# Kernel tuning notes

Measured on AMD Instinct MI355X. Metric: run time of the kernel, lower is better.

The kernel has to match this reference:

```python
import jax, jax.numpy as jnp
import numpy as np

# Config constants (match init_kwargs)
D_MODEL = 1024
N_EXPERTS = 8
EXPERT_SCALE = 2          # experts per base group -> n_base_groups = 4
N_FEAT = 16
BANK_DIM = 32
RAW_FEAT = N_FEAT * BANK_DIM   # 512
PROJ_DIM = 256
R_HIDDEN = 256
E_HIDDEN = 256
TOP_K = 2
TEMP = 1.0
LN_EPS = 1e-5


def _layernorm(x, g, b):
    mu = jnp.mean(x, axis=-1, keepdims=True)
    var = jnp.mean((x - mu) ** 2, axis=-1, keepdims=True)
    return (x - mu) * jax.lax.rsqrt(var + LN_EPS) * g + b


def _softmax_top_k(logits, k):
    # keep top-k logits, mask rest to -inf, softmax
    topv = jax.lax.top_k(logits, k)[0]
    thresh = topv[..., -1:]
    masked = jnp.where(logits >= thresh, logits, -jnp.inf)
    return jax.nn.softmax(masked, axis=-1)


def setup_inputs() -> dict:
    key = jax.random.key(0)
    ks = jax.random.split(key, 24)
    B, S = 4, 2048
    s = 0.02
    inp = {
        "hidden": jax.random.normal(ks[0], (B, S, D_MODEL), jnp.float32),
        "feat": jax.random.normal(ks[1], (B, S, N_FEAT), jnp.float32),
        "feat_bank": jax.random.normal(ks[2], (B, S, N_FEAT, BANK_DIM), jnp.float32),
        "item_seq_len": jax.random.randint(ks[3], (B,), 1, S + 1, jnp.int64),
        # pre-LN
        "ln_g": jnp.ones((D_MODEL,), jnp.float32),
        "ln_b": jnp.zeros((D_MODEL,), jnp.float32),
        # router feature projector (2 layers: Linear -> GELU -> Linear)
        "fp_w1": jax.random.normal(ks[4], (RAW_FEAT, PROJ_DIM), jnp.float32) * s,
        "fp_b1": jnp.zeros((PROJ_DIM,), jnp.float32),
        "fp_w2": jax.random.normal(ks[5], (PROJ_DIM, PROJ_DIM), jnp.float32) * s,
        "fp_b2": jnp.zeros((PROJ_DIM,), jnp.float32),
        # learned router MLP: d_in = d_model + proj_dim
        "r_w1": jax.random.normal(ks[6], (D_MODEL + PROJ_DIM, R_HIDDEN), jnp.float32) * s,
        "r_b1": jnp.zeros((R_HIDDEN,), jnp.float32),
        "r_w2": jax.random.normal(ks[7], (R_HIDDEN, N_EXPERTS), jnp.float32) * s,
        "r_b2": jnp.zeros((N_EXPERTS,), jnp.float32),
        # rule router (linear on raw stage features)
        "rr_w": jax.random.normal(ks[8], (N_FEAT, N_EXPERTS), jnp.float32) * s,
        "rr_b": jnp.zeros((N_EXPERTS,), jnp.float32),
        # per-expert FFN
        "e_w1": jax.random.normal(ks[9], (N_EXPERTS, D_MODEL, E_HIDDEN), jnp.float32) * s,
        "e_b1": jnp.zeros((N_EXPERTS, E_HIDDEN), jnp.float32),
        "e_w2": jax.random.normal(ks[10], (N_EXPERTS, E_HIDDEN, D_MODEL), jnp.float32) * s,
        "e_b2": jnp.zeros((N_EXPERTS, D_MODEL), jnp.float32),
        "alpha": jnp.ones((), jnp.float32),
    }
    return inp


def reference(hidden, feat, feat_bank, item_seq_len, ln_g, ln_b,
              fp_w1, fp_b1, fp_w2, fp_b2,
              r_w1, r_b1, r_w2, r_b2,
              rr_w, rr_b,
              e_w1, e_b1, e_w2, e_b2, alpha):
    B, S, D = hidden.shape
    h_norm = _layernorm(hidden, ln_g, ln_b)  # [B,S,D]

    # router feature path: flatten bank, 2-layer GELU projector
    bank_flat = feat_bank.reshape(B, S, RAW_FEAT)
    proj = jnp.dot(jax.nn.gelu(jnp.dot(bank_flat, fp_w1) + fp_b1), fp_w2) + fp_b2  # [B,S,P]

    # token-mode router input: concat hidden + projected features
    router_input = jnp.concatenate([h_norm, proj], axis=-1)
    rule_logits = jnp.dot(feat, rr_w) + rr_b  # rule router on raw stage features

    raw_logits = jnp.dot(jax.nn.gelu(jnp.dot(router_input, r_w1) + r_b1), r_w2) + r_b2
    scaled_logits = raw_logits / max(TEMP, 1e-6)
    gate_weights = _softmax_top_k(scaled_logits, TOP_K)           # [B,S,E]
    rule_target_logits = rule_logits / max(TEMP, 1e-6)

    # expert group: per-expert 2-layer GELU FFN on h_norm
    h1 = jax.nn.gelu(jnp.einsum('bsd,edh->bseh', h_norm, e_w1) + e_b1)
    expert_out = jnp.einsum('bseh,ehd->bsed', h1, e_w2) + e_b2    # [B,S,E,D]

    stage_out = jnp.einsum('bse,bsed->bsd', gate_weights, expert_out)
    next_hidden = hidden + alpha * stage_out

    # _aggregate_group_weights: expert_group_idx = arange(E)//EXPERT_SCALE is
    # contiguous, so gather+sum per group == reshape+sum over the scale axis
    n_groups = N_EXPERTS // EXPERT_SCALE
    group_weights = gate_weights.reshape(B, S, n_groups, EXPERT_SCALE).sum(-1)

    return (next_hidden, stage_out, gate_weights, scaled_logits, group_weights, rule_target_logits)
```

## Files before the change

kernel.cpp:

```cpp
#include <hip/hip_runtime.h>
#include <stdint.h>


typedef unsigned short u16;
using bf16x8 = __attribute__((ext_vector_type(8))) short;
using f32x4  = __attribute__((ext_vector_type(4))) float;

#define WS_HHI 0u
#define WS_HLO 16777216u
#define WS_PB2 33554432u
#define WS_W1T 67108864u
#define WS_IDX 71303168u
#define IX_SELE   0u
#define IX_SELG   65536u
#define IX_ROW    131072u
#define IX_TOKR   196608u
#define IX_GROW   262144u
#define IX_CNT    327680u
#define IX_CBASE  335872u
#define IX_TILEE  344064u
#define IX_TILES  344704u
#define IX_TILEC  345344u
#define IX_META   345984u
#define IX_TILEE2 346112u
#define IX_TILES2 347264u
#define IX_TILEC2 348416u

__device__ __forceinline__ float gelu_tanh(float x) {
  float x3 = x * x * x;
  float t = tanhf(0.7978845608028654f * (x + 0.044715f * x3));
  return 0.5f * x * (1.0f + t);
}
__device__ __forceinline__ u16 f2bf(float f) {
  uint32_t u = __float_as_uint(f);
  u = u + 0x7fffu + ((u >> 16) & 1u);
  return (u16)(u >> 16);
}
__device__ __forceinline__ float b2f(u16 h) {
  return __uint_as_float(((uint32_t)h) << 16);
}
__device__ __forceinline__ void gll16(const void* g, void* l) {
  __builtin_amdgcn_global_load_lds(
      (const __attribute__((address_space(1))) void*)g,
      (__attribute__((address_space(3))) void*)l, 16, 0, 0);
}

__global__ __launch_bounds__(256) void split_bank_kernel(const float* __restrict__ x,
    u16* __restrict__ hi, u16* __restrict__ lo) {
  int i4 = blockIdx.x * 256 + threadIdx.x;
  float4 v = ((const float4*)x)[i4];
  ushort4 h, l;
  h.x = f2bf(v.x); l.x = f2bf(v.x - b2f(h.x));
  h.y = f2bf(v.y); l.y = f2bf(v.y - b2f(h.y));
  h.z = f2bf(v.z); l.z = f2bf(v.z - b2f(h.z));
  h.w = f2bf(v.w); l.w = f2bf(v.w - b2f(h.w));
  ((ushort4*)hi)[i4] = h;
  ((ushort4*)lo)[i4] = l;
}

__global__ __launch_bounds__(256) void tsplit_kernel(const float* __restrict__ in,
    int inR, int inC, u16* __restrict__ outHi, u16* __restrict__ outLo,
    int outLD, int outColOff) {
  __shared__ u16 hs[64][65];
  __shared__ u16 ls[64][65];
  int tid = threadIdx.x;
  int c0 = blockIdx.x * 64, r0 = blockIdx.y * 64;
  const float* inp = in + (size_t)blockIdx.z * inR * inC;
  int rl = tid >> 6, cl = tid & 63;
#pragma unroll
  for (int p = 0; p < 16; p++) {
    int r = rl + p * 4;
    float v = inp[(size_t)(r0 + r) * inC + c0 + cl];
    u16 h = f2bf(v);
    hs[r][cl] = h;
    ls[r][cl] = f2bf(v - b2f(h));
  }
  __syncthreads();
  size_t obase = (size_t)(blockIdx.z * inC + c0) * outLD + outColOff + r0;
#pragma unroll
  for (int p = 0; p < 16; p++) {
    int c = rl + p * 4;
    outHi[obase + (size_t)c * outLD + cl] = hs[cl][c];
    if (outLo) outLo[obase + (size_t)c * outLD + cl] = ls[cl][c];
  }
}

__global__ __launch_bounds__(256) void wprime_kernel(const float* __restrict__ fp_w2,
    const float* __restrict__ r_w1, const float* __restrict__ fp_b2,
    const float* __restrict__ r_b1, float* __restrict__ wp, float* __restrict__ bp) {
  __shared__ float row[256];
  int i = blockIdx.x, n = threadIdx.x;
  if (i < 256) {
    row[n] = fp_w2[i * 256 + n];
    __syncthreads();
    float acc = 0.0f;
    for (int j = 0; j < 256; j++) acc += row[j] * r_w1[(size_t)(1024 + j) * 256 + n];
    wp[i * 256 + n] = acc;
  } else {
    row[n] = fp_b2[n];
    __syncthreads();
    float acc = r_b1[n];
    for (int j = 0; j < 256; j++) acc += row[j] * r_w1[(size_t)(1024 + j) * 256 + n];
    bp[n] = acc;
  }
}

__global__ __launch_bounds__(256) void ln_kernel(const float* __restrict__ hidden,
    const float* __restrict__ ln_g, const float* __restrict__ ln_b,
    const float* __restrict__ feat, const float* __restrict__ rr_w,
    const float* __restrict__ rr_b,
    u16* __restrict__ h_hi, u16* __restrict__ h_lo, float* __restrict__ rule) {
  int t = blockIdx.x;
  int tid = threadIdx.x;
  float4 v = ((const float4*)(hidden + (size_t)t * 1024))[tid];
  float s = v.x + v.y + v.z + v.w;
#pragma unroll
  for (int o = 32; o > 0; o >>= 1) s += __shfl_down(s, o);
  __shared__ float red[4];
  __shared__ float stats[2];
  int wid = tid >> 6, lane = tid & 63;
  if (lane == 0) red[wid] = s;
  __syncthreads();
  if (tid == 0) stats[0] = (red[0] + red[1] + red[2] + red[3]) * (1.0f / 1024.0f);
  __syncthreads();
  float mu = stats[0];
  float dx = v.x - mu, dy = v.y - mu, dz = v.z - mu, dw = v.w - mu;
  float q = dx * dx + dy * dy + dz * dz + dw * dw;
#pragma unroll
  for (int o = 32; o > 0; o >>= 1) q += __shfl_down(q, o);
  if (lane == 0) red[wid] = q;
  __syncthreads();
  if (tid == 0) {
    float var = (red[0] + red[1] + red[2] + red[3]) * (1.0f / 1024.0f) + 1e-5f;
    float r = rsqrtf(var);
    r = r * (1.5f - 0.5f * var * r * r);
    stats[1] = r;
  }
  __syncthreads();
  float r = stats[1];
  float4 g = ((const float4*)ln_g)[tid];
  float4 b = ((const float4*)ln_b)[tid];
  float4 o;
  o.x = dx * r * g.x + b.x;
  o.y = dy * r * g.y + b.y;
  o.z = dz * r * g.z + b.z;
  o.w = dw * r * g.w + b.w;
  ushort4 hv, lv;
  hv.x = f2bf(o.x); lv.x = f2bf(o.x - b2f(hv.x));
  hv.y = f2bf(o.y); lv.y = f2bf(o.y - b2f(hv.y));
  hv.z = f2bf(o.z); lv.z = f2bf(o.z - b2f(hv.z));
  hv.w = f2bf(o.w); lv.w = f2bf(o.w - b2f(hv.w));
  ((ushort4*)(h_hi + (size_t)t * 1024))[tid] = hv;
  ((ushort4*)(h_lo + (size_t)t * 1024))[tid] = lv;
  if (tid < 8) {
    float acc = rr_b[tid];
#pragma unroll
    for (int f = 0; f < 16; f++) acc += feat[t * 16 + f] * rr_w[f * 8 + tid];
    rule[t * 8 + tid] = acc;
  }
}

__global__ __launch_bounds__(256) void gemm3_kernel(
    const u16* __restrict__ Ah, const u16* __restrict__ Al, int lda,
    int kchunk, int nz1,
    const u16* __restrict__ A2h, const u16* __restrict__ A2l, int lda2,
    int klen2, int bkoff2,
    const u16* __restrict__ Bth, const u16* __restrict__ Btl, int Kb,
    float* __restrict__ parts) {
  __shared__ u16 Ash[128 * 32];
  __shared__ u16 Asl[128 * 32];
  __shared__ u16 Bsh[128 * 32];
  __shared__ u16 Bsl[128 * 32];
  int tid = threadIdx.x;
  int z = blockIdx.z;
  const u16 *pAh, *pAl;
  int lda_, akoff, bkoff, klen;
  if (z < nz1) {
    pAh = Ah; pAl = Al; lda_ = lda; akoff = z * kchunk; bkoff = akoff; klen = kchunk;
  } else {
    pAh = A2h; pAl = A2l; lda_ = lda2; akoff = 0; bkoff = bkoff2; klen = klen2;
  }
  int row0 = blockIdx.y * 128, col0 = blockIdx.x * 128;
  int wave = tid >> 6, lane = tid & 63;
  int wr = (wave >> 1) * 64, wc = (wave & 1) * 64;
  int l16 = lane & 15, qd = lane >> 4;
  f32x4 acc[4][4];
#pragma unroll
  for (int i = 0; i < 4; i++)
#pragma unroll
    for (int j = 0; j < 4; j++) acc[i][j] = 0.0f;

  int r0 = tid >> 2, kc = tid & 3;
  const u16* gAh0 = pAh + (size_t)(row0 + r0) * lda_ + akoff + kc * 8;
  const u16* gAh1 = gAh0 + (size_t)64 * lda_;
  const u16* gAl0 = pAl + (size_t)(row0 + r0) * lda_ + akoff + kc * 8;
  const u16* gAl1 = gAl0 + (size_t)64 * lda_;
  const u16* gBh0 = Bth + (size_t)(col0 + r0) * Kb + bkoff + kc * 8;
  const u16* gBh1 = gBh0 + (size_t)64 * Kb;
  const u16* gBl0 = Btl + (size_t)(col0 + r0) * Kb + bkoff + kc * 8;
  const u16* gBl1 = gBl0 + (size_t)64 * Kb;
  u16* dAh = Ash + tid * 8;
  u16* dAl = Asl + tid * 8;
  u16* dBh = Bsh + tid * 8;
  u16* dBl = Bsl + tid * 8;

  for (int k0 = 0; k0 < klen; k0 += 32) {
    __syncthreads();
    gll16(gAh0 + k0, dAh);
    gll16(gAh1 + k0, dAh + 2048);
    gll16(gAl0 + k0, dAl);
    gll16(gAl1 + k0, dAl + 2048);
    gll16(gBh0 + k0, dBh);
    gll16(gBh1 + k0, dBh + 2048);
    gll16(gBl0 + k0, dBl);
    gll16(gBl1 + k0, dBl + 2048);
    __syncthreads();
    bf16x8 afh[4], afl[4], bfh[4], bfl[4];
#pragma unroll
    for (int i = 0; i < 4; i++) {
      afh[i] = *((const bf16x8*)(Ash + (wr + i * 16 + l16) * 32 + qd * 8));
      afl[i] = *((const bf16x8*)(Asl + (wr + i * 16 + l16) * 32 + qd * 8));
      bfh[i] = *((const bf16x8*)(Bsh + (wc + i * 16 + l16) * 32 + qd * 8));
      bfl[i] = *((const bf16x8*)(Bsl + (wc + i * 16 + l16) * 32 + qd * 8));
    }
#pragma unroll
    for (int i = 0; i < 4; i++)
#pragma unroll
      for (int j = 0; j < 4; j++) {
        acc[i][j] = __builtin_amdgcn_mfma_f32_16x16x32_bf16(afh[i], bfh[j], acc[i][j], 0, 0, 0);
        acc[i][j] = __builtin_amdgcn_mfma_f32_16x16x32_bf16(afl[i], bfh[j], acc[i][j], 0, 0, 0);
        acc[i][j] = __builtin_amdgcn_mfma_f32_16x16x32_bf16(afh[i], bfl[j], acc[i][j], 0, 0, 0);
      }
  }

  float* pz = parts + (size_t)z * 2097152;
#pragma unroll
  for (int i = 0; i < 4; i++)
#pragma unroll
    for (int j = 0; j < 4; j++) {
      int cl = wc + j * 16 + l16;
#pragma unroll
      for (int rr = 0; rr < 4; rr++) {
        int rl = wr + i * 16 + qd * 4 + rr;
        pz[(size_t)(row0 + rl) * 256 + col0 + cl] = acc[i][j][rr];
      }
    }
}

__global__ __launch_bounds__(256) void epi_bf_kernel(const float* __restrict__ parts,
    int nz, const float* __restrict__ bias, int do_gelu,
    u16* __restrict__ hi, u16* __restrict__ lo) {
  int i4 = blockIdx.x * 256 + threadIdx.x;
  float4 s = ((const float4*)parts)[i4];
  for (int zz = 1; zz < nz; zz++) {
    float4 p = ((const float4*)parts)[(size_t)zz * 524288 + i4];
    s.x += p.x; s.y += p.y; s.z += p.z; s.w += p.w;
  }
  float4 bv = ((const float4*)bias)[i4 & 63];
  s.x += bv.x; s.y += bv.y; s.z += bv.z; s.w += bv.w;
  if (do_gelu) {
    s.x = gelu_tanh(s.x); s.y = gelu_tanh(s.y);
    s.z = gelu_tanh(s.z); s.w = gelu_tanh(s.w);
  }
  ushort4 h, l;
  h.x = f2bf(s.x); l.x = f2bf(s.x - b2f(h.x));
  h.y = f2bf(s.y); l.y = f2bf(s.y - b2f(h.y));
  h.z = f2bf(s.z); l.z = f2bf(s.z - b2f(h.z));
  h.w = f2bf(s.w); l.w = f2bf(s.w - b2f(h.w));
  ((ushort4*)hi)[i4] = h;
  ((ushort4*)lo)[i4] = l;
}

__global__ __launch_bounds__(256) void epi_f32_kernel(const float* __restrict__ parts,
    int nz, const float* __restrict__ bias, float* __restrict__ out) {
  int i4 = blockIdx.x * 256 + threadIdx.x;
  float4 s = ((const float4*)parts)[i4];
  for (int zz = 1; zz < nz; zz++) {
    float4 p = ((const float4*)parts)[(size_t)zz * 524288 + i4];
    s.x += p.x; s.y += p.y; s.z += p.z; s.w += p.w;
  }
  float4 bv = ((const float4*)bias)[i4 & 63];
  s.x = gelu_tanh(s.x + bv.x);
  s.y = gelu_tanh(s.y + bv.y);
  s.z = gelu_tanh(s.z + bv.z);
  s.w = gelu_tanh(s.w + bv.w);
  ((float4*)out)[i4] = s;
}

__global__ __launch_bounds__(256) void gate_kernel(const float* __restrict__ r1,
    const float* __restrict__ r_w2, const float* __restrict__ r_b2,
    float* __restrict__ gates, float* __restrict__ slog, float* __restrict__ gw,
    int* __restrict__ selE, float* __restrict__ selG, int* __restrict__ cnt) {
  __shared__ float w2s[2048];
  __shared__ float r1s[32][260];
  __shared__ float lg[32][8];
  __shared__ int se_s[64];
  int tid = threadIdx.x;
  int blk = blockIdx.x;
  int t0 = blk * 32;
  for (int i = tid; i < 2048; i += 256) {
    int e = i >> 8, k = i & 255;
    w2s[i] = r_w2[k * 8 + e];
  }
  for (int i = tid; i < 8192; i += 256) {
    int tt = i >> 8, k = i & 255;
    r1s[tt][k] = r1[(size_t)(t0 + tt) * 256 + k];
  }
  __syncthreads();
  {
    int tl = tid >> 3, e = tid & 7;
    float acc = r_b2[e];
    const float* wrp = &w2s[e * 256];
    const float* rrp = &r1s[tl][0];
    for (int k = 0; k < 256; k += 4) {
      float4 a = *(const float4*)(rrp + k);
      float4 b = *(const float4*)(wrp + k);
      acc += a.x * b.x + a.y * b.y + a.z * b.z + a.w * b.w;
    }
    lg[tl][e] = acc;
  }
  __syncthreads();
  if (tid < 32) {
    int t = t0 + tid;
    float l[8];
#pragma unroll
    for (int i = 0; i < 8; i++) l[i] = lg[tid][i];
    float m1 = -1e30f, m2 = -1e30f;
    int i1 = 0, i2 = 0;
#pragma unroll
    for (int i = 0; i < 8; i++) {
      float v = l[i];
      if (v > m1) { m2 = m1; i2 = i1; m1 = v; i1 = i; }
      else if (v > m2) { m2 = v; i2 = i; }
    }
    float w[8];
    float se = 0.0f;
#pragma unroll
    for (int i = 0; i < 8; i++) {
      float ex = (l[i] >= m2) ? expf(l[i] - m1) : 0.0f;
      w[i] = ex;
      se += ex;
    }
    float inv = 1.0f / se;
#pragma unroll
    for (int i = 0; i < 8; i++) {
      gates[(size_t)t * 8 + i] = w[i] * inv;
      slog[(size_t)t * 8 + i] = l[i];
    }
#pragma unroll
    for (int gi = 0; gi < 4; gi++)
      gw[(size_t)t * 4 + gi] = (w[2 * gi] + w[2 * gi + 1]) * inv;
    se_s[tid * 2] = i1;
    se_s[tid * 2 + 1] = i2;
    selE[t * 2] = i1;      selG[t * 2] = w[i1] * inv;
    selE[t * 2 + 1] = i2;  selG[t * 2 + 1] = w[i2] * inv;
  }
  __syncthreads();
  if (tid < 8) {
    int c = 0;
#pragma unroll
    for (int s = 0; s < 64; s++) c += (se_s[s] == tid) ? 1 : 0;
    cnt[blk * 8 + tid] = c;
  }
}

__global__ __launch_bounds__(256) void stageb_kernel(const int* __restrict__ cnt,
    int* __restrict__ cbase, int* __restrict__ tileE, int* __restrict__ tileS,
    int* __restrict__ tileC, int* __restrict__ tileE2, int* __restrict__ tileS2,
    int* __restrict__ tileC2, int* __restrict__ meta) {
  __shared__ int cs[2048];
  __shared__ int tot[8];
  __shared__ int ebase[8];
  int tid = threadIdx.x;
  for (int i = tid; i < 2048; i += 256) cs[i] = cnt[i];
  __syncthreads();
  if (tid < 8) {
    int s = 0;
    for (int c = 0; c < 256; c++) s += cs[c * 8 + tid];
    tot[tid] = s;
  }
  __syncthreads();
  if (tid == 0) {
    int b = 0, nt = 0;
    for (int e = 0; e < 8; e++) {
      ebase[e] = b;
      int c = tot[e];
      for (int off = 0; off < c; off += 128) {
        tileE[nt] = e; tileS[nt] = b + off;
        tileC[nt] = (c - off < 128) ? (c - off) : 128;
        nt++;
      }
      b += c;
    }
    meta[16] = nt;
    int b2 = 0, nt2 = 0;
    for (int e = 0; e < 8; e++) {
      int c = tot[e];
      for (int off = 0; off < c; off += 64) {
        tileE2[nt2] = e; tileS2[nt2] = b2 + off;
        tileC2[nt2] = (c - off < 64) ? (c - off) : 64;
        nt2++;
      }
      b2 += c;
    }
    meta[17] = nt2;
  }
  __syncthreads();
  if (tid < 8) {
    int run = ebase[tid];
    for (int c = 0; c < 256; c++) {
      cbase[c * 8 + tid] = run;
      run += cs[c * 8 + tid];
    }
  }
}

__global__ __launch_bounds__(256) void scatter_kernel(const int* __restrict__ selE,
    const float* __restrict__ selG, const int* __restrict__ cbase,
    int* __restrict__ rowsel, int* __restrict__ tokrow, float* __restrict__ grow) {
  int chunk = blockIdx.x;
  int wave = threadIdx.x >> 6, lane = threadIdx.x & 63;
  int slot = chunk * 64 + lane;
  int sel = selE[slot];
  float g = selG[slot];
  int tokn = chunk * 32 + (lane >> 1);
  unsigned long long lt = (1ULL << lane) - 1ULL;
#pragma unroll
  for (int ei = 0; ei < 2; ei++) {
    int e = wave + ei * 4;
    unsigned long long m = __ballot(sel == e);
    if (sel == e) {
      int row = cbase[chunk * 8 + e] + __popcll(m & lt);
      rowsel[slot] = row;
      tokrow[row] = tokn;
      grow[row] = g;
    }
  }
}

__global__ __launch_bounds__(256) void gexp1_kernel(const u16* __restrict__ A,
    const u16* __restrict__ w1t, const float* __restrict__ e_b1,
    const int* __restrict__ tokrow, const float* __restrict__ grow,
    const int* __restrict__ tileE2, const int* __restrict__ tileS2,
    const int* __restrict__ tileC2, const int* __restrict__ meta,
    u16* __restrict__ pb1) {
  __shared__ u16 As0[64 * 32];
  __shared__ u16 As1[64 * 32];
  __shared__ u16 Bs0[64 * 32];
  __shared__ u16 Bs1[64 * 32];
  __shared__ float gsl[64];
  int n = blockIdx.x;
  int ty = ((n >> 5) << 3) + (n & 7);
  int cblk = (n >> 3) & 3;
  if (ty >= meta[17]) return;
  int e = tileE2[ty], pstart = tileS2[ty], pcnt = tileC2[ty];
  int tid = threadIdx.x;
  int col0 = cblk * 64;
  if (tid < 64) {
    int rr = (tid < pcnt) ? tid : (pcnt - 1);
    gsl[tid] = grow[pstart + rr];
  }
  int wave = tid >> 6, lane = tid & 63;
  int wr = (wave >> 1) * 32, wc = (wave & 1) * 32;
  int l16 = lane & 15, qd = lane >> 4;
  int xq = qd ^ ((l16 >> 1) & 3);
  f32x4 acc[2][2];
  acc[0][0] = 0.0f; acc[0][1] = 0.0f; acc[1][0] = 0.0f; acc[1][1] = 0.0f;

  int r0 = tid >> 2, kc = tid & 3;
  int kcs = kc ^ ((r0 >> 1) & 3);
  int ra = (r0 < pcnt) ? r0 : (pcnt - 1);
  int ta = tokrow[pstart + ra];
  const u16* Ap = A + (size_t)ta * 1024 + kcs * 8;
  const u16* Bp = w1t + (size_t)(e * 256 + col0 + r0) * 1024 + kcs * 8;
  u16* dA0 = As0 + tid * 8;
  u16* dA1 = As1 + tid * 8;
  u16* dB0 = Bs0 + tid * 8;
  u16* dB1 = Bs1 + tid * 8;

  int aoff0 = (wr + l16) * 32 + xq * 8;
  int aoff1 = aoff0 + 16 * 32;
  int boff0 = (wc + l16) * 32 + xq * 8;
  int boff1 = boff0 + 16 * 32;

  gll16(Ap, dA0);
  gll16(Bp, dB0);
  __syncthreads();

  for (int k0 = 0; k0 < 1024; k0 += 64) {
    {
      gll16(Ap + k0 + 32, dA1);
      gll16(Bp + k0 + 32, dB1);
      bf16x8 a0 = *((const bf16x8*)(As0 + aoff0));
      bf16x8 a1 = *((const bf16x8*)(As0 + aoff1));
      bf16x8 b0 = *((const bf16x8*)(Bs0 + boff0));
      bf16x8 b1 = *((const bf16x8*)(Bs0 + boff1));
      acc[0][0] = __builtin_amdgcn_mfma_f32_16x16x32_bf16(a0, b0, acc[0][0], 0, 0, 0);
      acc[0][1] = __builtin_amdgcn_mfma_f32_16x16x32_bf16(a0, b1, acc[0][1], 0, 0, 0);
      acc[1][0] = __builtin_amdgcn_mfma_f32_16x16x32_bf16(a1, b0, acc[1][0], 0, 0, 0);
      acc[1][1] = __builtin_amdgcn_mfma_f32_16x16x32_bf16(a1, b1, acc[1][1], 0, 0, 0);
      __syncthreads();
    }
    {
      if (k0 + 64 < 1024) {
        gll16(Ap + k0 + 64, dA0);
        gll16(Bp + k0 + 64, dB0);
      }
      bf16x8 a0 = *((const bf16x8*)(As1 + aoff0));
      bf16x8 a1 = *((const bf16x8*)(As1 + aoff1));
      bf16x8 b0 = *((const bf16x8*)(Bs1 + boff0));
      bf16x8 b1 = *((const bf16x8*)(Bs1 + boff1));
      acc[0][0] = __builtin_amdgcn_mfma_f32_16x16x32_bf16(a0, b0, acc[0][0], 0, 0, 0);
      acc[0][1] = __builtin_amdgcn_mfma_f32_16x16x32_bf16(a0, b1, acc[0][1], 0, 0, 0);
      acc[1][0] = __builtin_amdgcn_mfma_f32_16x16x32_bf16(a1, b0, acc[1][0], 0, 0, 0);
      acc[1][1] = __builtin_amdgcn_mfma_f32_16x16x32_bf16(a1, b1, acc[1][1], 0, 0, 0);
      __syncthreads();
    }
  }

#pragma unroll
  for (int i = 0; i < 2; i++)
#pragma unroll
    for (int j = 0; j < 2; j++) {
      int cl = wc + j * 16 + l16;
      int col = col0 + cl;
      float bc = e_b1[e * 256 + col];
#pragma unroll
      for (int rr = 0; rr < 4; rr++) {
        int rl = wr + i * 16 + qd * 4 + rr;
        if (rl < pcnt) {
          float v = gelu_tanh(acc[i][j][rr] + bc) * gsl[rl];
          pb1[(size_t)(pstart + rl) * 256 + col] = f2bf(v);
        }
      }
    }
}

__global__ __launch_bounds__(256) void gexp2_kernel(const u16* __restrict__ pb1,
    const u16* __restrict__ w2te,
    const int* __restrict__ tileE, const int* __restrict__ tileS,
    const int* __restrict__ tileC, const int* __restrict__ meta,
    u16* __restrict__ pb2) {
  int ty = blockIdx.y;
  if (ty >= meta[16]) return;
  int e = tileE[ty], pstart = tileS[ty], pcnt = tileC[ty];
  if (pcnt <= 0) return;
  __shared__ u16 As[128 * 32];
  __shared__ u16 Bs[128 * 32];
  int tid = threadIdx.x;
  int col0 = blockIdx.x * 128;
  int wave = tid >> 6, lane = tid & 63;
  int wr = (wave >> 1) * 64, wc = (wave & 1) * 64;
  int l16 = lane & 15, qd = lane >> 4;
  f32x4 acc[4][4];
#pragma unroll
  for (int i = 0; i < 4; i++)
#pragma unroll
    for (int j = 0; j < 4; j++) acc[i][j] = 0.0f;

  int r0 = tid >> 2, kc = tid & 3;
  int ra = (r0 < pcnt) ? r0 : (pcnt - 1);
  int rb = (r0 + 64 < pcnt) ? (r0 + 64) : (pcnt - 1);
  const u16* Ap0 = pb1 + (size_t)(pstart + ra) * 256 + kc * 8;
  const u16* Ap1 = pb1 + (size_t)(pstart + rb) * 256 + kc * 8;
  const u16* Bp0 = w2te + (size_t)(e * 1024 + col0 + r0) * 256 + kc * 8;
  const u16* Bp1 = Bp0 + (size_t)64 * 256;
  u16* dA = As + tid * 8;
  u16* dB = Bs + tid * 8;

  for (int k0 = 0; k0 < 256; k0 += 32) {
    __syncthreads();
    gll16(Ap0 + k0, dA);
    gll16(Ap1 + k0, dA + 2048);
    gll16(Bp0 + k0, dB);
    gll16(Bp1 + k0, dB + 2048);
    __syncthreads();
    bf16x8 af[4], bfr[4];
#pragma unroll
    for (int i = 0; i < 4; i++) {
      af[i]  = *((const bf16x8*)(As + (wr + i * 16 + l16) * 32 + qd * 8));
      bfr[i] = *((const bf16x8*)(Bs + (wc + i * 16 + l16) * 32 + qd * 8));
    }
#pragma unroll
    for (int i = 0; i < 4; i++)
#pragma unroll
      for (int j = 0; j < 4; j++)
        acc[i][j] = __builtin_amdgcn_mfma_f32_16x16x32_bf16(af[i], bfr[j], acc[i][j], 0, 0, 0);
  }

#pragma unroll
  for (int i = 0; i < 4; i++)
#pragma unroll
    for (int j = 0; j < 4; j++) {
      int cl = wc + j * 16 + l16;
#pragma unroll
      for (int rr = 0; rr < 4; rr++) {
        int rl = wr + i * 16 + qd * 4 + rr;
        if (rl < pcnt)
          pb2[(size_t)(pstart + rl) * 1024 + col0 + cl] = f2bf(acc[i][j][rr]);
      }
    }
}

__global__ __launch_bounds__(256) void combine_kernel(const u16* __restrict__ pb2,
    const int* __restrict__ rowsel, const int* __restrict__ selE,
    const float* __restrict__ selG, const float* __restrict__ e_b2,
    const float* __restrict__ hidden, const float* __restrict__ alpha_p,
    float* __restrict__ stage, float* __restrict__ next) {
  int t = blockIdx.x;
  int c = threadIdx.x * 4;
  int rA = rowsel[t * 2], rB = rowsel[t * 2 + 1];
  int eA = selE[t * 2], eB = selE[t * 2 + 1];
  float gA = selG[t * 2], gB = selG[t * 2 + 1];
  float al = alpha_p[0];
  ushort4 pa = *((const ushort4*)(pb2 + (size_t)rA * 1024 + c));
  ushort4 pb = *((const ushort4*)(pb2 + (size_t)rB * 1024 + c));
  float4 ba = *((const float4*)(e_b2 + (size_t)eA * 1024 + c));
  float4 bb = *((const float4*)(e_b2 + (size_t)eB * 1024 + c));
  float4 h = *((const float4*)(hidden + (size_t)t * 1024 + c));
  float4 v;
  v.x = b2f(pa.x) + b2f(pb.x) + gA * ba.x + gB * bb.x;
  v.y = b2f(pa.y) + b2f(pb.y) + gA * ba.y + gB * bb.y;
  v.z = b2f(pa.z) + b2f(pb.z) + gA * ba.z + gB * bb.z;
  v.w = b2f(pa.w) + b2f(pb.w) + gA * ba.w + gB * bb.w;
  *((float4*)(stage + (size_t)t * 1024 + c)) = v;
  float4 n;
  n.x = h.x + al * v.x; n.y = h.y + al * v.y;
  n.z = h.z + al * v.z; n.w = h.w + al * v.w;
  *((float4*)(next + (size_t)t * 1024 + c)) = n;
}

extern "C" void kernel_launch(void* const* d_in, const int* in_sizes, int n_in,
                              void* d_out, int out_size, void* d_ws, size_t ws_size,
                              hipStream_t stream) {
  const float* hidden    = (const float*)d_in[0];
  const float* feat      = (const float*)d_in[1];
  const float* feat_bank = (const float*)d_in[2];
  const float* ln_g  = (const float*)d_in[4];
  const float* ln_b  = (const float*)d_in[5];
  const float* fp_w1 = (const float*)d_in[6];
  const float* fp_b1 = (const float*)d_in[7];
  const float* fp_w2 = (const float*)d_in[8];
  const float* fp_b2 = (const float*)d_in[9];
  const float* r_w1  = (const float*)d_in[10];
  const float* r_b1  = (const float*)d_in[11];
  const float* r_w2  = (const float*)d_in[12];
  const float* r_b2  = (const float*)d_in[13];
  const float* rr_w  = (const float*)d_in[14];
  const float* rr_b  = (const float*)d_in[15];
  const float* e_w1  = (const float*)d_in[16];
  const float* e_b1  = (const float*)d_in[17];
  const float* e_w2  = (const float*)d_in[18];
  const float* e_b2  = (const float*)d_in[19];
  const float* alpha = (const float*)d_in[20];

  char* ob = (char*)d_out;
  float* next  = (float*)ob;
  float* stage = (float*)(ob + 33554432);
  float* gates = (float*)(ob + 67108864);
  float* slog  = gates + 65536;
  float* gw    = slog + 65536;
  float* rule  = gw + 32768;

  u16* bank_hi  = (u16*)ob;
  u16* bank_lo  = (u16*)(ob + 8388608);
  float* r1     = (float*)ob;
  u16* fpw1t_hi = (u16*)(ob + 16777216);
  u16* fpw1t_lo = (u16*)(ob + 17039360);
  float* wp     = (float*)(ob + 17301504);
  float* bp     = (float*)(ob + 17563648);
  u16* rw1t_hi  = (u16*)(ob + 17825792);
  u16* rw1t_lo  = (u16*)(ob + 18481152);
  u16* mid_hi   = (u16*)(ob + 19136512);
  u16* mid_lo   = (u16*)(ob + 23330816);
  u16* w2te     = (u16*)(ob + 19136512);

  char* sb = ob + 33554432;
  float* parts = (float*)sb;
  u16* pb1     = (u16*)sb;

  char* ws = (char*)d_ws;
  u16* h_hi = (u16*)(ws + WS_HHI);
  u16* h_lo = (u16*)(ws + WS_HLO);
  u16* pb2  = (u16*)(ws + WS_PB2);
  u16* w1t  = (u16*)(ws + WS_W1T);
  char* ix  = ws + WS_IDX;
  int*   selE   = (int*)(ix + IX_SELE);
  float* selG   = (float*)(ix + IX_SELG);
  int*   rowsel = (int*)(ix + IX_ROW);
  int*   tokrow = (int*)(ix + IX_TOKR);
  float* grow   = (float*)(ix + IX_GROW);
  int*   cnt    = (int*)(ix + IX_CNT);
  int*   cbase  = (int*)(ix + IX_CBASE);
  int*   tileE  = (int*)(ix + IX_TILEE);
  int*   tileS  = (int*)(ix + IX_TILES);
  int*   tileC  = (int*)(ix + IX_TILEC);
  int*   tileE2 = (int*)(ix + IX_TILEE2);
  int*   tileS2 = (int*)(ix + IX_TILES2);
  int*   tileC2 = (int*)(ix + IX_TILEC2);
  int*   meta   = (int*)(ix + IX_META);

  split_bank_kernel<<<4096, 256, 0, stream>>>(feat_bank, bank_hi, bank_lo);
  wprime_kernel<<<257, 256, 0, stream>>>(fp_w2, r_w1, fp_b2, r_b1, wp, bp);
  tsplit_kernel<<<dim3(4, 8, 1), 256, 0, stream>>>(fp_w1, 512, 256,
      fpw1t_hi, fpw1t_lo, 512, 0);
  tsplit_kernel<<<dim3(4, 16, 1), 256, 0, stream>>>(r_w1, 1024, 256,
      rw1t_hi, rw1t_lo, 1280, 0);
  tsplit_kernel<<<dim3(4, 4, 1), 256, 0, stream>>>(wp, 256, 256,
      rw1t_hi, rw1t_lo, 1280, 1024);
  tsplit_kernel<<<dim3(4, 16, 8), 256, 0, stream>>>(e_w1, 1024, 256,
      w1t, nullptr, 1024, 0);
  ln_kernel<<<8192, 256, 0, stream>>>(hidden, ln_g, ln_b, feat, rr_w, rr_b,
                                      h_hi, h_lo, rule);
  gemm3_kernel<<<dim3(2, 64, 4), 256, 0, stream>>>(
      bank_hi, bank_lo, 512, 128, 4,
      bank_hi, bank_lo, 512, 0, 0,
      fpw1t_hi, fpw1t_lo, 512, parts);
  epi_bf_kernel<<<2048, 256, 0, stream>>>(parts, 4, fp_b1, 1, mid_hi, mid_lo);
  gemm3_kernel<<<dim3(2, 64, 3), 256, 0, stream>>>(
      h_hi, h_lo, 1024, 512, 2,
      mid_hi, mid_lo, 256, 256, 1024,
      rw1t_hi, rw1t_lo, 1280, parts);
  tsplit_kernel<<<dim3(16, 4, 8), 256, 0, stream>>>(e_w2, 256, 1024,
      w2te, nullptr, 256, 0);
  epi_f32_kernel<<<2048, 256, 0, stream>>>(parts, 3, bp, r1);
  gate_kernel<<<256, 256, 0, stream>>>(r1, r_w2, r_b2, gates, slog, gw,
      selE, selG, cnt);
  stageb_kernel<<<1, 256, 0, stream>>>(cnt, cbase, tileE, tileS, tileC,
      tileE2, tileS2, tileC2, meta);
  scatter_kernel<<<256, 256, 0, stream>>>(selE, selG, cbase, rowsel, tokrow, grow);
  gexp1_kernel<<<1152, 256, 0, stream>>>(h_hi, w1t, e_b1, tokrow, grow,
      tileE2, tileS2, tileC2, meta, pb1);
  gexp2_kernel<<<dim3(8, 136), 256, 0, stream>>>(pb1, w2te, tileE, tileS, tileC,
      meta, pb2);
  combine_kernel<<<8192, 256, 0, stream>>>(pb2, rowsel, selE, selG, e_b2,
      hidden, alpha, stage, next);
}
```

Baseline: 356.0 us.

## Double-buffer LDS tiles and XOR-swizzle layout in gemm3 and gexp2 kernels

Two GEMM kernels now use ping-pong shared-memory buffers so that the global-to-LDS load of the next K slice is issued before the MFMA compute on the current slice. This removes one barrier per iteration and the load stall. The K-chunk column index is also XOR-swizzled by row on both the store and read side, to reduce LDS bank conflicts on the bf16x8 fragment reads. LDS usage doubles (64KB for gemm3), which may reduce occupancy. The loop also assumes klen is a multiple of 64.

New measurement: 354.6 us. About the same (-0.4%).

```diff
diff --git a/kernel.cpp b/kernel.cpp
--- a/kernel.cpp
+++ b/kernel.cpp
@@ -160,6 +160,33 @@
   }
 }
 
+#define G3_STAGE(K, AH, AL, BH, BL)          \
+  gll16(gAh0 + (K), AH + tid * 8);           \
+  gll16(gAh1 + (K), AH + tid * 8 + 2048);    \
+  gll16(gAl0 + (K), AL + tid * 8);           \
+  gll16(gAl1 + (K), AL + tid * 8 + 2048);    \
+  gll16(gBh0 + (K), BH + tid * 8);           \
+  gll16(gBh1 + (K), BH + tid * 8 + 2048);    \
+  gll16(gBl0 + (K), BL + tid * 8);           \
+  gll16(gBl1 + (K), BL + tid * 8 + 2048);
+
+#define G3_COMPUTE(AH, AL, BH, BL)                                             \
+  {                                                                            \
+    bf16x8 afh[4], afl[4], bfh[4], bfl[4];                                     \
+    _Pragma("unroll") for (int i = 0; i < 4; i++) {                            \
+      afh[i] = *((const bf16x8*)(AH + (wr + i * 16 + l16) * 32 + xq * 8));     \
+      afl[i] = *((const bf16x8*)(AL + (wr + i * 16 + l16) * 32 + xq * 8));     \
+      bfh[i] = *((const bf16x8*)(BH + (wc + i * 16 + l16) * 32 + xq * 8));     \
+      bfl[i] = *((const bf16x8*)(BL + (wc + i * 16 + l16) * 32 + xq * 8));     \
+    }                                                                          \
+    _Pragma("unroll") for (int i = 0; i < 4; i++)                              \
+      _Pragma("unroll") for (int j = 0; j < 4; j++) {                          \
+        acc[i][j] = __builtin_amdgcn_mfma_f32_16x16x32_bf16(afh[i], bfh[j], acc[i][j], 0, 0, 0); \
+        acc[i][j] = __builtin_amdgcn_mfma_f32_16x16x32_bf16(afl[i], bfh[j], acc[i][j], 0, 0, 0); \
+        acc[i][j] = __builtin_amdgcn_mfma_f32_16x16x32_bf16(afh[i], bfl[j], acc[i][j], 0, 0, 0); \
+      }                                                                        \
+  }
+
 __global__ __launch_bounds__(256) void gemm3_kernel(
     const u16* __restrict__ Ah, const u16* __restrict__ Al, int lda,
     int kchunk, int nz1,
@@ -167,10 +194,10 @@
     int klen2, int bkoff2,
     const u16* __restrict__ Bth, const u16* __restrict__ Btl, int Kb,
     float* __restrict__ parts) {
-  __shared__ u16 Ash[128 * 32];
-  __shared__ u16 Asl[128 * 32];
-  __shared__ u16 Bsh[128 * 32];
-  __shared__ u16 Bsl[128 * 32];
+  __shared__ u16 Ash0[4096], Ash1[4096];
+  __shared__ u16 Asl0[4096], Asl1[4096];
+  __shared__ u16 Bsh0[4096], Bsh1[4096];
+  __shared__ u16 Bsl0[4096], Bsl1[4096];
   int tid = threadIdx.x;
   int z = blockIdx.z;
   const u16 *pAh, *pAl;
@@ -184,6 +211,7 @@
   int wave = tid >> 6, lane = tid & 63;
   int wr = (wave >> 1) * 64, wc = (wave & 1) * 64;
   int l16 = lane & 15, qd = lane >> 4;
+  int xq = qd ^ ((l16 >> 1) & 3);
   f32x4 acc[4][4];
 #pragma unroll
   for (int i = 0; i < 4; i++)
@@ -191,46 +219,27 @@
     for (int j = 0; j < 4; j++) acc[i][j] = 0.0f;
 
   int r0 = tid >> 2, kc = tid & 3;
-  const u16* gAh0 = pAh + (size_t)(row0 + r0) * lda_ + akoff + kc * 8;
+  int kcs = kc ^ ((r0 >> 1) & 3);
+  const u16* gAh0 = pAh + (size_t)(row0 + r0) * lda_ + akoff + kcs * 8;
   const u16* gAh1 = gAh0 + (size_t)64 * lda_;
-  const u16* gAl0 = pAl + (size_t)(row0 + r0) * lda_ + akoff + kc * 8;
+  const u16* gAl0 = pAl + (size_t)(row0 + r0) * lda_ + akoff + kcs * 8;
   const u16* gAl1 = gAl0 + (size_t)64 * lda_;
-  const u16* gBh0 = Bth + (size_t)(col0 + r0) * Kb + bkoff + kc * 8;
+  const u16* gBh0 = Bth + (size_t)(col0 + r0) * Kb + bkoff + kcs * 8;
   const u16* gBh1 = gBh0 + (size_t)64 * Kb;
-  const u16* gBl0 = Btl + (size_t)(col0 + r0) * Kb + bkoff + kc * 8;
+  const u16* gBl0 = Btl + (size_t)(col0 + r0) * Kb + bkoff + kcs * 8;
   const u16* gBl1 = gBl0 + (size_t)64 * Kb;
-  u16* dAh = Ash + tid * 8;
-  u16* dAl = Asl + tid * 8;
-  u16* dBh = Bsh + tid * 8;
-  u16* dBl = Bsl + tid * 8;
-
-  for (int k0 = 0; k0 < klen; k0 += 32) {
+
+  G3_STAGE(0, Ash0, Asl0, Bsh0, Bsl0);
+  __syncthreads();
+  for (int k0 = 0; k0 < klen; k0 += 64) {
+    G3_STAGE(k0 + 32, Ash1, Asl1, Bsh1, Bsl1);
+    G3_COMPUTE(Ash0, Asl0, Bsh0, Bsl0);
     __syncthreads();
-    gll16(gAh0 + k0, dAh);
-    gll16(gAh1 + k0, dAh + 2048);
-    gll16(gAl0 + k0, dAl);
-    gll16(gAl1 + k0, dAl + 2048);
-    gll16(gBh0 + k0, dBh);
-    gll16(gBh1 + k0, dBh + 2048);
-    gll16(gBl0 + k0, dBl);
-    gll16(gBl1 + k0, dBl + 2048);
+    if (k0 + 64 < klen) {
+      G3_STAGE(k0 + 64, Ash0, Asl0, Bsh0, Bsl0);
+    }
+    G3_COMPUTE(Ash1, Asl1, Bsh1, Bsl1);
     __syncthreads();
-    bf16x8 afh[4], afl[4], bfh[4], bfl[4];
-#pragma unroll
-    for (int i = 0; i < 4; i++) {
-      afh[i] = *((const bf16x8*)(Ash + (wr + i * 16 + l16) * 32 + qd * 8));
-      afl[i] = *((const bf16x8*)(Asl + (wr + i * 16 + l16) * 32 + qd * 8));
-      bfh[i] = *((const bf16x8*)(Bsh + (wc + i * 16 + l16) * 32 + qd * 8));
-      bfl[i] = *((const bf16x8*)(Bsl + (wc + i * 16 + l16) * 32 + qd * 8));
-    }
-#pragma unroll
-    for (int i = 0; i < 4; i++)
-#pragma unroll
-      for (int j = 0; j < 4; j++) {
-        acc[i][j] = __builtin_amdgcn_mfma_f32_16x16x32_bf16(afh[i], bfh[j], acc[i][j], 0, 0, 0);
-        acc[i][j] = __builtin_amdgcn_mfma_f32_16x16x32_bf16(afl[i], bfh[j], acc[i][j], 0, 0, 0);
-        acc[i][j] = __builtin_amdgcn_mfma_f32_16x16x32_bf16(afh[i], bfl[j], acc[i][j], 0, 0, 0);
-      }
   }
 
   float* pz = parts + (size_t)z * 2097152;
@@ -536,6 +545,24 @@
     }
 }
 
+#define GX2_STAGE(K, AS, BS)              \
+  gll16(Ap0 + (K), AS + tid * 8);         \
+  gll16(Ap1 + (K), AS + tid * 8 + 2048);  \
+  gll16(Bp0 + (K), BS + tid * 8);         \
+  gll16(Bp1 + (K), BS + tid * 8 + 2048);
+
+#define GX2_COMPUTE(AS, BS)                                                   \
+  {                                                                           \
+    bf16x8 af[4], bfr[4];                                                     \
+    _Pragma("unroll") for (int i = 0; i < 4; i++) {                           \
+      af[i]  = *((const bf16x8*)(AS + (wr + i * 16 + l16) * 32 + xq * 8));    \
+      bfr[i] = *((const bf16x8*)(BS + (wc + i * 16 + l16) * 32 + xq * 8));    \
+    }                                                                         \
+    _Pragma("unroll") for (int i = 0; i < 4; i++)                             \
+      _Pragma("unroll") for (int j = 0; j < 4; j++)                           \
+        acc[i][j] = __builtin_amdgcn_mfma_f32_16x16x32_bf16(af[i], bfr[j], acc[i][j], 0, 0, 0); \
+  }
+
 __global__ __launch_bounds__(256) void gexp2_kernel(const u16* __restrict__ pb1,
     const u16* __restrict__ w2te,
     const int* __restrict__ tileE, const int* __restrict__ tileS,
@@ -545,13 +572,14 @@
   if (ty >= meta[16]) return;
   int e = tileE[ty], pstart = tileS[ty], pcnt = tileC[ty];
   if (pcnt <= 0) return;
-  __shared__ u16 As[128 * 32];
-  __shared__ u16 Bs[128 * 32];
+  __shared__ u16 As0[4096], As1[4096];
+  __shared__ u16 Bs0[4096], Bs1[4096];
   int tid = threadIdx.x;
   int col0 = blockIdx.x * 128;
   int wave = tid >> 6, lane = tid & 63;
   int wr = (wave >> 1) * 64, wc = (wave & 1) * 64;
   int l16 = lane & 15, qd = lane >> 4;
+  int xq = qd ^ ((l16 >> 1) & 3);
   f32x4 acc[4][4];
 #pragma unroll
   for (int i = 0; i < 4; i++)
@@ -559,33 +587,25 @@
     for (int j = 0; j < 4; j++) acc[i][j] = 0.0f;
 
   int r0 = tid >> 2, kc = tid & 3;
+  int kcs = kc ^ ((r0 >> 1) & 3);
   int ra = (r0 < pcnt) ? r0 : (pcnt - 1);
   int rb = (r0 + 64 < pcnt) ? (r0 + 64) : (pcnt - 1);
-  const u16* Ap0 = pb1 + (size_t)(pstart + ra) * 256 + kc * 8;
-  const u16* Ap1 = pb1 + (size_t)(pstart + rb) * 256 + kc * 8;
-  const u16* Bp0 = w2te + (size_t)(e * 1024 + col0 + r0) * 256 + kc * 8;
+  const u16* Ap0 = pb1 + (size_t)(pstart + ra) * 256 + kcs * 8;
+  const u16* Ap1 = pb1 + (size_t)(pstart + rb) * 256 + kcs * 8;
+  const u16* Bp0 = w2te + (size_t)(e * 1024 + col0 + r0) * 256 + kcs * 8;
   const u16* Bp1 = Bp0 + (size_t)64 * 256;
-  u16* dA = As + tid * 8;
-  u16* dB = Bs + tid * 8;
-
-  for (int k0 = 0; k0 < 256; k0 += 32) {
+
+  GX2_STAGE(0, As0, Bs0);
+  __syncthreads();
+  for (int k0 = 0; k0 < 256; k0 += 64) {
+    GX2_STAGE(k0 + 32, As1, Bs1);
+    GX2_COMPUTE(As0, Bs0);
     __syncthreads();
-    gll16(Ap0 + k0, dA);
-    gll16(Ap1 + k0, dA + 2048);
-    gll16(Bp0 + k0, dB);
-    gll16(Bp1 + k0, dB + 2048);
+    if (k0 + 64 < 256) {
+      GX2_STAGE(k0 + 64, As0, Bs0);
+    }
+    GX2_COMPUTE(As1, Bs1);
     __syncthreads();
-    bf16x8 af[4], bfr[4];
-#pragma unroll
-    for (int i = 0; i < 4; i++) {
-      af[i]  = *((const bf16x8*)(As + (wr + i * 16 + l16) * 32 + qd * 8));
-      bfr[i] = *((const bf16x8*)(Bs + (wc + i * 16 + l16) * 32 + qd * 8));
-    }
-#pragma unroll
-    for (int i = 0; i < 4; i++)
-#pragma unroll
-      for (int j = 0; j < 4; j++)
-        acc[i][j] = __builtin_amdgcn_mfma_f32_16x16x32_bf16(af[i], bfr[j], acc[i][j], 0, 0, 0);
   }
 
 #pragma unroll
```
